# Optimization experiments

Measured on AMD Instinct MI355X. Metric: run time of the kernel, lower is better.

## Reference

```python
import jax, jax.numpy as jnp
import numpy as np

ITERATIONS = 20


def _affine_sample(canvas, theta):
    """PyTorch-equivalent F.affine_grid + F.grid_sample (bilinear,
    align_corners=False, padding_mode='zeros') for all T transforms at once.
    canvas: [H, W], theta: [T, 2, 3] -> returns [T, H, W].
    """
    H, W = canvas.shape
    dt = canvas.dtype
    # Normalized base grid coords, align_corners=False: centers of pixels.
    xs = (jnp.arange(W, dtype=dt) * 2 + 1) / W - 1  # [W]
    ys = (jnp.arange(H, dtype=dt) * 2 + 1) / H - 1  # [H]
    # Sampled normalized coords: [x', y'] = theta @ [x, y, 1]
    gx = (theta[:, 0, 0, None, None] * xs[None, None, :]
          + theta[:, 0, 1, None, None] * ys[None, :, None]
          + theta[:, 0, 2, None, None])  # [T, H, W]
    gy = (theta[:, 1, 0, None, None] * xs[None, None, :]
          + theta[:, 1, 1, None, None] * ys[None, :, None]
          + theta[:, 1, 2, None, None])  # [T, H, W]
    # Unnormalize to pixel coords (align_corners=False).
    ix = (gx + 1) * (W * 0.5) - 0.5
    iy = (gy + 1) * (H * 0.5) - 0.5
    x0f = jnp.floor(ix)
    y0f = jnp.floor(iy)
    wx1 = ix - x0f
    wy1 = iy - y0f
    wx0 = 1 - wx1
    wy0 = 1 - wy1
    x0 = x0f.astype(jnp.int32)
    y0 = y0f.astype(jnp.int32)

    def corner(xi, yi):
        valid = (xi >= 0) & (xi < W) & (yi >= 0) & (yi < H)
        v = canvas[jnp.clip(yi, 0, H - 1), jnp.clip(xi, 0, W - 1)]
        return jnp.where(valid, v, jnp.zeros((), dt))  # zeros padding

    return (wx0 * wy0 * corner(x0, y0)
            + wx1 * wy0 * corner(x0 + 1, y0)
            + wx0 * wy1 * corner(x0, y0 + 1)
            + wx1 * wy1 * corner(x0 + 1, y0 + 1))


def setup_inputs() -> dict:
    key = jax.random.key(0)
    k1, k2, k3 = jax.random.split(key, 3)
    H, W, T = 1024, 1024, 16
    canvas0 = jax.random.uniform(k1, (H, W), dtype=jnp.float32)
    theta = jax.random.normal(k2, (T, 2, 3), dtype=jnp.float32)
    probs = jax.random.uniform(k3, (T,), dtype=jnp.float32)
    base_value = jnp.zeros((1,), dtype=jnp.float32)
    return {"canvas0": canvas0, "theta": theta, "probs": probs,
            "base_value": base_value}


def reference(canvas0, theta, probs, base_value):
    p = probs / jnp.sum(probs)

    def step(canvas, _):
        sampled = _affine_sample(canvas, theta)          # [T, H, W]
        new_canvas = jnp.einsum('t,thw->hw', p, sampled)  # weighted IFS sum
        return new_canvas, None

    canvas, _ = jax.lax.scan(step, canvas0, None, length=ITERATIONS)
    return canvas + base_value[0]
```

## Files before the change

kernel.cpp:

```cpp
#include <hip/hip_runtime.h>

constexpr int W = 1024;
constexpr int H = 1024;
constexpr int T = 16;
constexpr int ITERS = 20;
constexpr int PITCH = 1040;
constexpr int PH = H + 2;
constexpr int PAD_ELEMS = PH * PITCH;
constexpr int TILES_X = W / 16;
constexpr int TILES_Y = H / 16;

typedef float f2 __attribute__((ext_vector_type(2), aligned(4)));

__global__ void setup_coef(const float* __restrict__ theta,
                           const float* __restrict__ probs,
                           float* __restrict__ coef) {
    int t = threadIdx.x;
    if (t >= T) return;
    float sum = 0.f;
    for (int i = 0; i < T; ++i) sum += probs[i];
    float p = probs[t] / sum;
    const float* th = theta + 6 * t;
    float a = th[0], b = th[1], c = th[2];
    float d = th[3], e = th[4], f = th[5];
    float Cx = a * ((1.0f - (float)W) * 0.5f)
             + b * ((1.0f - (float)H) * 0.5f)
             + (c + 1.0f) * ((float)W * 0.5f) - 0.5f;
    float Cy = d * ((1.0f - (float)W) * 0.5f)
             + e * ((1.0f - (float)H) * 0.5f)
             + (f + 1.0f) * ((float)H * 0.5f) - 0.5f;
    float* o = coef + 8 * t;
    o[0] = p;  o[1] = a;  o[2] = b;  o[3] = Cx + 1.0f;
    o[4] = d;  o[5] = e;  o[6] = Cy + 1.0f; o[7] = 0.f;
}

__global__ __launch_bounds__(256) void setup_mask(const float* __restrict__ coef,
                                                  unsigned* __restrict__ mask) {
    int tile = blockIdx.x * 256 + threadIdx.x;
    if (tile >= TILES_X * TILES_Y) return;
    int tx = tile & (TILES_X - 1), ty = tile / TILES_X;
    float w0 = (float)(tx * 16), w1 = w0 + 15.f;
    float h0 = (float)(ty * 16), h1 = h0 + 15.f;
    unsigned m = 0;
    for (int t = 0; t < T; ++t) {
        float Ax = coef[t * 8 + 1], Bx = coef[t * 8 + 2], Cx = coef[t * 8 + 3];
        float Ay = coef[t * 8 + 4], By = coef[t * 8 + 5], Cy = coef[t * 8 + 6];
        float ixmin = Cx + (Ax >= 0.f ? Ax * w0 : Ax * w1) + (Bx >= 0.f ? Bx * h0 : Bx * h1);
        float ixmax = Cx + (Ax >= 0.f ? Ax * w1 : Ax * w0) + (Bx >= 0.f ? Bx * h1 : Bx * h0);
        float iymin = Cy + (Ay >= 0.f ? Ay * w0 : Ay * w1) + (By >= 0.f ? By * h0 : By * h1);
        float iymax = Cy + (Ay >= 0.f ? Ay * w1 : Ay * w0) + (By >= 0.f ? By * h1 : By * h0);
        bool hit = !(ixmax <= 0.f || ixmin >= (float)(W + 1) ||
                     iymax <= 0.f || iymin >= (float)(H + 1));
        if (hit) m |= (1u << t);
    }
    mask[tile] = m;
}

__global__ __launch_bounds__(256) void copy_in(const float* __restrict__ src,
                                               float* __restrict__ dst) {
    int i = blockIdx.x * 256 + threadIdx.x;
    int h = i >> 10, w = i & 1023;
    dst[(h + 1) * PITCH + (w + 1)] = src[i];
}

__global__ __launch_bounds__(256) void ifs_iter(const float* __restrict__ in,
                                                float* __restrict__ out,
                                                const float* __restrict__ coef,
                                                const unsigned* __restrict__ mask,
                                                const float* __restrict__ base,
                                                int dstPitch, int dstOff,
                                                int add_base) {
    __shared__ float sc[(T + 3) * 8];

    unsigned tmask = mask[blockIdx.y * TILES_X + blockIdx.x];
    int nact = __popc(tmask);
    int lid = threadIdx.x;

    if (lid < T * 8) {
        int t = lid >> 3;
        if (tmask & (1u << t)) {
            int pos = __popc(tmask & ((1u << t) - 1));
            sc[pos * 8 + (lid & 7)] = coef[lid];
        }
    }
    if (lid < 24) sc[nact * 8 + lid] = 0.f;
    __syncthreads();

    int lane = lid & 63;
    int wv   = lid >> 6;
    int w = blockIdx.x * 16 + ((wv & 1) << 3) + (lane & 7);
    int h = blockIdx.y * 16 + ((wv >> 1) << 3) + (lane >> 3);
    float wf = (float)w, hf = (float)h;

    float acc = 0.f;

    for (int g = 0; g < nact; g += 4) {
        const float* c = sc + g * 8;
        float fx[4], fy[4], pe[4];
        int id0[4];
#pragma unroll
        for (int k = 0; k < 4; ++k) {
            const float* ck = c + k * 8;
            float p = ck[0], Ax = ck[1], Bx = ck[2], Cx = ck[3];
            float Ay = ck[4], By = ck[5], Cy = ck[6];
            float x = fmaf(Ax, wf, fmaf(Bx, hf, Cx));
            float y = fmaf(Ay, wf, fmaf(By, hf, Cy));
            float xf = floorf(x), yf = floorf(y);
            bool act = (xf >= 0.f) & (xf <= (float)W) & (yf >= 0.f) & (yf <= (float)H);
            id0[k] = act ? (int)fmaf(yf, (float)PITCH, xf) : 0;
            pe[k]  = act ? p : 0.f;
            fx[k] = x - xf;
            fy[k] = y - yf;
        }
        f2 r0[4], r1[4];
#pragma unroll
        for (int k = 0; k < 4; ++k) {
            r0[k] = *(const f2*)(in + id0[k]);
            r1[k] = *(const f2*)(in + id0[k] + PITCH);
        }
#pragma unroll
        for (int k = 0; k < 4; ++k) {
            float top = fmaf(fx[k], r0[k].y - r0[k].x, r0[k].x);
            float bot = fmaf(fx[k], r1[k].y - r1[k].x, r1[k].x);
            acc = fmaf(pe[k], fmaf(fy[k], bot - top, top), acc);
        }
    }

    if (add_base) acc += base[0];
    out[h * dstPitch + w + dstOff] = acc;
}

extern "C" void kernel_launch(void* const* d_in, const int* in_sizes, int n_in,
                              void* d_out, int out_size, void* d_ws, size_t ws_size,
                              hipStream_t stream) {
    const float* canvas0 = (const float*)d_in[0];
    const float* theta   = (const float*)d_in[1];
    const float* probs   = (const float*)d_in[2];
    const float* base    = (const float*)d_in[3];
    float* out = (float*)d_out;

    float* bufA = (float*)d_ws;
    float* bufB = bufA + PAD_ELEMS;
    float* coef = bufB + PAD_ELEMS;
    unsigned* mask = (unsigned*)(coef + T * 8);

    hipMemsetAsync(d_ws, 0, (size_t)2 * PAD_ELEMS * sizeof(float), stream);

    setup_coef<<<1, 64, 0, stream>>>(theta, probs, coef);
    setup_mask<<<(TILES_X * TILES_Y + 255) / 256, 256, 0, stream>>>(coef, mask);
    copy_in<<<(H * W) / 256, 256, 0, stream>>>(canvas0, bufA);

    dim3 block(256);
    dim3 grid(TILES_X, TILES_Y);

    const float* cur = bufA;
    for (int i = 0; i < ITERS; ++i) {
        bool last = (i == ITERS - 1);
        float* dst = last ? out : ((i & 1) ? bufA : bufB);
        int dstPitch = last ? W : PITCH;
        int dstOff   = last ? 0 : (PITCH + 1);
        ifs_iter<<<grid, block, 0, stream>>>(cur, dst, coef, mask, base,
                                             dstPitch, dstOff, last ? 1 : 0);
        cur = dst;
    }
}
```

Before: 416.4 us.

## Skip transforms whose source footprint covers only all-zero tiles from prior iteration

After: 457.7 us. +9.9%, slower.

```diff
diff --git a/kernel.cpp b/kernel.cpp
--- a/kernel.cpp
+++ b/kernel.cpp
@@ -9,6 +9,7 @@
 constexpr int PAD_ELEMS = PH * PITCH;
 constexpr int TILES_X = W / 16;
 constexpr int TILES_Y = H / 16;
+constexpr int NTILES = TILES_X * TILES_Y;
 
 typedef float f2 __attribute__((ext_vector_type(2), aligned(4)));
 
@@ -34,28 +35,6 @@
     o[4] = d;  o[5] = e;  o[6] = Cy + 1.0f; o[7] = 0.f;
 }
 
-__global__ __launch_bounds__(256) void setup_mask(const float* __restrict__ coef,
-                                                  unsigned* __restrict__ mask) {
-    int tile = blockIdx.x * 256 + threadIdx.x;
-    if (tile >= TILES_X * TILES_Y) return;
-    int tx = tile & (TILES_X - 1), ty = tile / TILES_X;
-    float w0 = (float)(tx * 16), w1 = w0 + 15.f;
-    float h0 = (float)(ty * 16), h1 = h0 + 15.f;
-    unsigned m = 0;
-    for (int t = 0; t < T; ++t) {
-        float Ax = coef[t * 8 + 1], Bx = coef[t * 8 + 2], Cx = coef[t * 8 + 3];
-        float Ay = coef[t * 8 + 4], By = coef[t * 8 + 5], Cy = coef[t * 8 + 6];
-        float ixmin = Cx + (Ax >= 0.f ? Ax * w0 : Ax * w1) + (Bx >= 0.f ? Bx * h0 : Bx * h1);
-        float ixmax = Cx + (Ax >= 0.f ? Ax * w1 : Ax * w0) + (Bx >= 0.f ? Bx * h1 : Bx * h0);
-        float iymin = Cy + (Ay >= 0.f ? Ay * w0 : Ay * w1) + (By >= 0.f ? By * h0 : By * h1);
-        float iymax = Cy + (Ay >= 0.f ? Ay * w1 : Ay * w0) + (By >= 0.f ? By * h1 : By * h0);
-        bool hit = !(ixmax <= 0.f || ixmin >= (float)(W + 1) ||
-                     iymax <= 0.f || iymin >= (float)(H + 1));
-        if (hit) m |= (1u << t);
-    }
-    mask[tile] = m;
-}
-
 __global__ __launch_bounds__(256) void copy_in(const float* __restrict__ src,
                                                float* __restrict__ dst) {
     int i = blockIdx.x * 256 + threadIdx.x;
@@ -66,28 +45,66 @@
 __global__ __launch_bounds__(256) void ifs_iter(const float* __restrict__ in,
                                                 float* __restrict__ out,
                                                 const float* __restrict__ coef,
-                                                const unsigned* __restrict__ mask,
+                                                const int* __restrict__ maskIn,
+                                                int* __restrict__ maskOut,
                                                 const float* __restrict__ base,
                                                 int dstPitch, int dstOff,
                                                 int add_base) {
     __shared__ float sc[(T + 3) * 8];
+    __shared__ int sn;
 
-    unsigned tmask = mask[blockIdx.y * TILES_X + blockIdx.x];
-    int nact = __popc(tmask);
-    int lid = threadIdx.x;
-
-    if (lid < T * 8) {
-        int t = lid >> 3;
-        if (tmask & (1u << t)) {
-            int pos = __popc(tmask & ((1u << t) - 1));
-            sc[pos * 8 + (lid & 7)] = coef[lid];
-        }
-    }
-    if (lid < 24) sc[nact * 8 + lid] = 0.f;
-    __syncthreads();
-
+    int lid  = threadIdx.x;
     int lane = lid & 63;
     int wv   = lid >> 6;
+
+    if (wv == 0) {
+        bool act = false;
+        float cc[8] = {0, 0, 0, 0, 0, 0, 0, 0};
+        if (lane < T) {
+            const float* c = coef + lane * 8;
+#pragma unroll
+            for (int j = 0; j < 8; ++j) cc[j] = c[j];
+            float Ax = cc[1], Bx = cc[2], Cx = cc[3];
+            float Ay = cc[4], By = cc[5], Cy = cc[6];
+            float w0 = (float)(blockIdx.x * 16), w1 = w0 + 15.f;
+            float h0 = (float)(blockIdx.y * 16), h1 = h0 + 15.f;
+            float ixmin = Cx + (Ax >= 0.f ? Ax * w0 : Ax * w1) + (Bx >= 0.f ? Bx * h0 : Bx * h1);
+            float ixmax = Cx + (Ax >= 0.f ? Ax * w1 : Ax * w0) + (Bx >= 0.f ? Bx * h1 : Bx * h0);
+            float iymin = Cy + (Ay >= 0.f ? Ay * w0 : Ay * w1) + (By >= 0.f ? By * h0 : By * h1);
+            float iymax = Cy + (Ay >= 0.f ? Ay * w1 : Ay * w0) + (By >= 0.f ? By * h1 : By * h0);
+            bool hit = (ixmax > 0.f) & (ixmin < 1025.f) & (iymax > 0.f) & (iymin < 1025.f);
+            if (hit) {
+                float xlo = fmaxf(floorf(ixmin) - 1.f, 0.f);
+                float xhi = fminf(floorf(ixmax) + 2.f, 1025.f);
+                float ylo = fmaxf(floorf(iymin) - 1.f, 0.f);
+                float yhi = fminf(floorf(iymax) + 2.f, 1025.f);
+                int ux0 = max((int)xlo - 1, 0), ux1 = min((int)xhi - 1, 1023);
+                int uy0 = max((int)ylo - 1, 0), uy1 = min((int)yhi - 1, 1023);
+                int tx0 = ux0 >> 4, tx1 = ux1 >> 4;
+                int ty0 = uy0 >> 4, ty1 = uy1 >> 4;
+                int nt = (tx1 - tx0 + 1) * (ty1 - ty0 + 1);
+                if (nt > 64) {
+                    act = true;
+                } else {
+                    for (int ty = ty0; ty <= ty1 && !act; ++ty)
+                        for (int tx = tx0; tx <= tx1; ++tx)
+                            if (maskIn[ty * TILES_X + tx]) { act = true; break; }
+                }
+            }
+        }
+        unsigned long long bal = __ballot(act);
+        int nact = __popcll(bal);
+        if (act) {
+            int pos = __popcll(bal & ((1ull << lane) - 1ull));
+#pragma unroll
+            for (int j = 0; j < 8; ++j) sc[pos * 8 + j] = cc[j];
+        }
+        if (lane >= 40) sc[nact * 8 + (lane - 40)] = 0.f;
+        if (lane == 0) sn = nact;
+    }
+    __syncthreads();
+    int nact = sn;
+
     int w = blockIdx.x * 16 + ((wv & 1) << 3) + (lane & 7);
     int h = blockIdx.y * 16 + ((wv >> 1) << 3) + (lane >> 3);
     float wf = (float)w, hf = (float)h;
@@ -126,6 +143,9 @@
         }
     }
 
+    int any = __syncthreads_or(acc != 0.f ? 1 : 0);
+    if (lid == 0) maskOut[blockIdx.y * TILES_X + blockIdx.x] = any;
+
     if (add_base) acc += base[0];
     out[h * dstPitch + w + dstOff] = acc;
 }
@@ -142,12 +162,13 @@
     float* bufA = (float*)d_ws;
     float* bufB = bufA + PAD_ELEMS;
     float* coef = bufB + PAD_ELEMS;
-    unsigned* mask = (unsigned*)(coef + T * 8);
+    int* maskP0 = (int*)(coef + T * 8);
+    int* maskP1 = maskP0 + NTILES;
 
     hipMemsetAsync(d_ws, 0, (size_t)2 * PAD_ELEMS * sizeof(float), stream);
+    hipMemsetAsync(maskP1, 0xFF, NTILES * sizeof(int), stream);
 
     setup_coef<<<1, 64, 0, stream>>>(theta, probs, coef);
-    setup_mask<<<(TILES_X * TILES_Y + 255) / 256, 256, 0, stream>>>(coef, mask);
     copy_in<<<(H * W) / 256, 256, 0, stream>>>(canvas0, bufA);
 
     dim3 block(256);
@@ -159,7 +180,9 @@
         float* dst = last ? out : ((i & 1) ? bufA : bufB);
         int dstPitch = last ? W : PITCH;
         int dstOff   = last ? 0 : (PITCH + 1);
-        ifs_iter<<<grid, block, 0, stream>>>(cur, dst, coef, mask, base,
+        const int* mIn = ((i + 1) & 1) ? maskP1 : maskP0;
+        int*       mOut = (i & 1) ? maskP1 : maskP0;
+        ifs_iter<<<grid, block, 0, stream>>>(cur, dst, coef, mIn, mOut, base,
                                              dstPitch, dstOff, last ? 1 : 0);
         cur = dst;
     }
```
